# Kernel optimization log

Hardware: AMD Instinct MI355X
Metric: run time of the kernel (lower is better)

The kernel has to match this reference:

```python
import jax, jax.numpy as jnp
import numpy as np

B, CIN, COUT, H, W = 8, 256, 256, 64, 64
K, STRIDE, PAD = 3, 1, 1


def setup_inputs() -> dict:
    key = jax.random.key(0)
    k1, k2, k3 = jax.random.split(key, 3)
    x = jax.random.normal(k1, (B, CIN, H, W), dtype=jnp.float32)
    offset = jax.random.normal(k2, (B, 2 * K * K, H, W), dtype=jnp.float32)
    weight = jax.random.normal(k3, (COUT, CIN, K, K), dtype=jnp.float32) * 0.05
    return {"x": x, "offset": offset, "weight": weight}


def _deform_conv2d(x, offset, weight):
    # x: [B, C, H, W]; offset: [B, 2*K*K, Ho, Wo] (y,x interleaved per tap, mmcv layout)
    Bn, C, Hh, Ww = x.shape
    Ho, Wo = Hh, Ww  # stride=1, pad=1, k=3
    K2 = K * K
    ki, kj = jnp.meshgrid(jnp.arange(K), jnp.arange(K), indexing="ij")
    ki = ki.reshape(-1).astype(jnp.float32)  # [K2] row offset of tap
    kj = kj.reshape(-1).astype(jnp.float32)
    hh = jnp.arange(Ho, dtype=jnp.float32)
    ww = jnp.arange(Wo, dtype=jnp.float32)
    # base sampling grid per tap: [K2, Ho, Wo]
    base_y = ki[:, None, None] + hh[None, :, None] * STRIDE - PAD
    base_x = kj[:, None, None] + ww[None, None, :] * STRIDE - PAD
    off = offset.reshape(Bn, K2, 2, Ho, Wo)
    py = base_y[None] + off[:, :, 0]  # [B, K2, Ho, Wo]
    px = base_x[None] + off[:, :, 1]

    y0 = jnp.floor(py)
    x0 = jnp.floor(px)

    def gather(im, yy, xx):
        # im: [C, H, W]; yy, xx: [K2, Ho, Wo] -> [C, K2, Ho, Wo]
        return im[:, yy, xx]

    vgather = jax.vmap(gather)  # over batch

    val = jnp.zeros((Bn, C, K2, Ho, Wo), dtype=x.dtype)
    for dy in (0.0, 1.0):
        for dx in (0.0, 1.0):
            yi = y0 + dy
            xi = x0 + dx
            wgt = (1.0 - jnp.abs(py - yi)) * (1.0 - jnp.abs(px - xi))
            valid = (yi >= 0) & (yi < Hh) & (xi >= 0) & (xi < Ww)
            yc = jnp.clip(yi, 0, Hh - 1).astype(jnp.int32)
            xc = jnp.clip(xi, 0, Ww - 1).astype(jnp.int32)
            v = vgather(x, yc, xc)  # [B, C, K2, Ho, Wo]
            val = val + v * (wgt * valid)[:, None]

    w2 = weight.reshape(weight.shape[0], C, K2)
    return jnp.einsum("bckhw,ock->bohw", val, w2)


def reference(x, offset, weight):
    return jax.nn.relu(_deform_conv2d(x, offset, weight))
```

## Files before the change

### kernel.cpp

```cpp
#include <hip/hip_runtime.h>


#define B_   8
#define C_   256
#define H_   64
#define W_   64
#define K2_  9
#define HW_  4096
#define NC4  64

typedef __fp16 f16x2 __attribute__((ext_vector_type(2)));
typedef __fp16 f16x8 __attribute__((ext_vector_type(8)));
typedef float  f32x4 __attribute__((ext_vector_type(4)));

static __device__ __forceinline__ f16x2 u2h(unsigned u) {
    union { unsigned u; f16x2 h; } v; v.u = u; return v.h;
}
static __device__ __forceinline__ unsigned h2u(f16x2 h) {
    union { unsigned u; f16x2 h; } v; v.h = h; return v.u;
}

__global__ __launch_bounds__(256) void pack_kernel(
    const float* __restrict__ x, const float* __restrict__ w,
    uint4* __restrict__ xpt, unsigned short* __restrict__ wA)
{
    const int tid = threadIdx.x;
    if (blockIdx.x >= 512) {
        const int t = (blockIdx.x - 512) * 256 + tid;
        if (t < C_ * C_ * K2_) {
            const int k = t % 9;
            const int c = (t / 9) & 255;
            const int o = t / (9 * 256);
            const int cc = c >> 5, lg = (c >> 3) & 3, e = c & 7;
            const int t16 = o >> 4, lr = o & 15;
            const int dst = e + 8 * (lr + 16 * (lg + 4 * (t16 + 16 * (cc + 8 * k))));
            const __fp16 h = (__fp16)w[t];
            unsigned short us;
            __builtin_memcpy(&us, &h, 2);
            wA[dst] = us;
        }
        return;
    }
    const int bid = blockIdx.x;
    const int b = bid >> 6, y = bid & 63;
    __shared__ unsigned pr[64][256];
    const float* xb = x + ((size_t)(b * C_ + tid) * H_ + y) * W_;
#pragma unroll
    for (int i = 0; i < 16; ++i) {
        const int c0 = i * 4;
        const float4 v = *(const float4*)(xb + c0);
        const float nxt = xb[(c0 == 60) ? 63 : c0 + 4];
        pr[c0 + 0][tid] = h2u(__builtin_amdgcn_cvt_pkrtz(v.x, v.y));
        pr[c0 + 1][tid] = h2u(__builtin_amdgcn_cvt_pkrtz(v.y, v.z));
        pr[c0 + 2][tid] = h2u(__builtin_amdgcn_cvt_pkrtz(v.z, v.w));
        pr[c0 + 3][tid] = h2u(__builtin_amdgcn_cvt_pkrtz(v.w, nxt));
    }
    __syncthreads();
    const int lane = tid & 63, wv = tid >> 6;
    uint4* dst = xpt + ((size_t)b * HW_ + (size_t)y * 64) * NC4;
#pragma unroll
    for (int i = 0; i < 16; ++i) {
        const int col = wv * 16 + i;
        dst[(size_t)col * NC4 + lane] = *(const uint4*)&pr[col][lane * 4];
    }
}

template<int MODE>
__global__ __launch_bounds__(512, 2) void deform_main(
    const float* __restrict__ x, const uint4* __restrict__ xpt,
    const float* __restrict__ offset, const unsigned short* __restrict__ wA,
    float* __restrict__ out)
{
    extern __shared__ char smem[];
    unsigned short (*btile)[128][256] =
        (unsigned short (*)[128][256])smem;
    uint2*          gw2   = (uint2*)(smem + 131072);
    unsigned short* gaddr = (unsigned short*)(smem + 140288);

    const int bid = blockIdx.x;
    const int b = bid & 7, ho2 = bid >> 3;
    const int tid = threadIdx.x;
    const int lane = tid & 63;
    const int wv   = tid >> 6;
    const int lr = lane & 15, lg = (lane >> 4) & 3;

    for (int e = tid; e < K2_ * 128; e += 512) {
        const int k = e >> 7, p = e & 127;
        const int row = p >> 6, wo = p & 63;
        const int ho = ho2 * 2 + row;
        const float offy = offset[((b * 18 + 2 * k    ) * H_ + ho) * W_ + wo];
        const float offx = offset[((b * 18 + 2 * k + 1) * H_ + ho) * W_ + wo];
        const float py = (float)(k / 3 + ho - 1) + offy;
        const float px = (float)(k % 3 + wo - 1) + offx;
        const float y0f = floorf(py), x0f = floorf(px);
        const int   y0 = (int)y0f,   x0 = (int)x0f;
        const float fy = py - y0f,   fx = px - x0f;
        const float wy0 = (y0 >= 0  && y0 < H_)     ? 1.f - fy : 0.f;
        const float wy1 = (y0 >= -1 && y0 < H_ - 1) ? fy       : 0.f;
        const float wx0 = (x0 >= 0  && x0 < W_)     ? 1.f - fx : 0.f;
        const float wx1 = (x0 >= -1 && x0 < W_ - 1) ? fx       : 0.f;
        const int ys = min(max(y0, 0), H_ - 2);
        const int xs = min(max(x0, 0), W_ - 2);
        const float qy0 = (ys == y0 ? wy0 : 0.f) + (ys == y0 + 1 ? wy1 : 0.f);
        const float qy1 = (ys + 1 == y0 ? wy0 : 0.f) + (ys + 1 == y0 + 1 ? wy1 : 0.f);
        const float qx0 = (xs == x0 ? wx0 : 0.f) + (xs == x0 + 1 ? wx1 : 0.f);
        const float qx1 = (xs + 1 == x0 ? wx0 : 0.f) + (xs + 1 == x0 + 1 ? wx1 : 0.f);
        gaddr[k * 128 + p] = (unsigned short)(ys * W_ + xs);
        gw2[k * 128 + p] = make_uint2(
            h2u(__builtin_amdgcn_cvt_pkrtz(qy0 * qx0, qy0 * qx1)),
            h2u(__builtin_amdgcn_cvt_pkrtz(qy1 * qx0, qy1 * qx1)));
    }
    __syncthreads();

    f32x4 acc[2][8];
#pragma unroll
    for (int m = 0; m < 2; ++m)
#pragma unroll
        for (int n = 0; n < 8; ++n) acc[m][n] = (f32x4)0.f;

    const __fp16* wAh = (const __fp16*)wA;
    const uint4* xptb = xpt + (size_t)b * HW_ * NC4;

#define A_LOAD(k_, cc_, AS, AT) {                                              \
    const __fp16* ap_ = wAh +                                                  \
        (((size_t)((k_) * 8 + (cc_)) * 16 + wv * 2) * 64 + lane) * 8;          \
    AS = *(const f16x8*)ap_;                                                   \
    AT = *(const f16x8*)(ap_ + 512); }

#define G_ISSUE(t_, j_, QT, QB) {                                              \
    const int qp_ = gaddr[(t_) * 128 + wv * 16 + (j_)];                        \
    QT = xptb[(size_t)qp_ * NC4 + lane];                                       \
    QB = xptb[(size_t)(qp_ + 64) * NC4 + lane]; }

#define G_CONSUME(t_, j_, QT, QB, SB) {                                        \
    const int p_ = wv * 16 + (j_);                                             \
    const uint2 wp_ = gw2[(t_) * 128 + p_];                                    \
    const f16x2 wt_ = u2h(wp_.x), wb_ = u2h(wp_.y);                            \
    const float v0_ = __builtin_amdgcn_fdot2(u2h(QT.x), wt_,                   \
        __builtin_amdgcn_fdot2(u2h(QB.x), wb_, 0.f, false), false);            \
    const float v1_ = __builtin_amdgcn_fdot2(u2h(QT.y), wt_,                   \
        __builtin_amdgcn_fdot2(u2h(QB.y), wb_, 0.f, false), false);            \
    const float v2_ = __builtin_amdgcn_fdot2(u2h(QT.z), wt_,                   \
        __builtin_amdgcn_fdot2(u2h(QB.z), wb_, 0.f, false), false);            \
    const float v3_ = __builtin_amdgcn_fdot2(u2h(QT.w), wt_,                   \
        __builtin_amdgcn_fdot2(u2h(QB.w), wb_, 0.f, false), false);            \
    const unsigned pk0_ = h2u(__builtin_amdgcn_cvt_pkrtz(v0_, v1_));           \
    const unsigned pk1_ = h2u(__builtin_amdgcn_cvt_pkrtz(v2_, v3_));           \
    const int phys_ = (lane >> 1) ^ (p_ & 7);                                  \
    *(uint2*)((char*)&btile[SB][p_][0] + phys_ * 16 + (lane & 1) * 8) =        \
        make_uint2(pk0_, pk1_); }

#define MFMA_CC(cc_, MB, AS, AT) {                                             \
    _Pragma("unroll")                                                          \
    for (int nt = 0; nt < 8; ++nt) {                                           \
        const int pix_ = nt * 16 + lr;                                         \
        const int phys_ = ((cc_) * 4 + lg) ^ (pix_ & 7);                       \
        const f16x8 bv_ = *(const f16x8*)                                      \
            ((const char*)&btile[MB][pix_][0] + phys_ * 16);                   \
        acc[0][nt] = __builtin_amdgcn_mfma_f32_16x16x32_f16(                   \
            AS, bv_, acc[0][nt], 0, 0, 0);                                     \
        acc[1][nt] = __builtin_amdgcn_mfma_f32_16x16x32_f16(                   \
            AT, bv_, acc[1][nt], 0, 0, 0);                                     \
    } }

#define G_ISSUE_8(t_)                                                          \
    G_ISSUE(t_, 0, qT0, qB0) G_ISSUE(t_, 1, qT1, qB1)                          \
    G_ISSUE(t_, 2, qT2, qB2) G_ISSUE(t_, 3, qT3, qB3)                          \
    G_ISSUE(t_, 4, qT4, qB4) G_ISSUE(t_, 5, qT5, qB5)                          \
    G_ISSUE(t_, 6, qT6, qB6) G_ISSUE(t_, 7, qT7, qB7)

    if constexpr (MODE == 0) {
        uint4 qT0, qB0, qT1, qB1, qT2, qB2, qT3, qB3;
        uint4 qT4, qB4, qT5, qB5, qT6, qB6, qT7, qB7;
        f16x8 aS0, aT0, aS1, aT1, aS2, aT2, aS3, aT3;

        A_LOAD(0, 0, aS0, aT0)
        A_LOAD(0, 1, aS1, aT1)
        G_ISSUE_8(0)
        G_CONSUME(0, 0, qT0, qB0, 0)  G_ISSUE(0, 8, qT0, qB0)
        G_CONSUME(0, 1, qT1, qB1, 0)  G_ISSUE(0, 9, qT1, qB1)
        G_CONSUME(0, 2, qT2, qB2, 0)  G_ISSUE(0, 10, qT2, qB2)
        G_CONSUME(0, 3, qT3, qB3, 0)  G_ISSUE(0, 11, qT3, qB3)
        G_CONSUME(0, 4, qT4, qB4, 0)  G_ISSUE(0, 12, qT4, qB4)
        G_CONSUME(0, 5, qT5, qB5, 0)  G_ISSUE(0, 13, qT5, qB5)
        G_CONSUME(0, 6, qT6, qB6, 0)  G_ISSUE(0, 14, qT6, qB6)
        G_CONSUME(0, 7, qT7, qB7, 0)  G_ISSUE(0, 15, qT7, qB7)
        G_CONSUME(0, 8, qT0, qB0, 0)  G_CONSUME(0, 9, qT1, qB1, 0)
        G_CONSUME(0, 10, qT2, qB2, 0) G_CONSUME(0, 11, qT3, qB3, 0)
        G_CONSUME(0, 12, qT4, qB4, 0) G_CONSUME(0, 13, qT5, qB5, 0)
        G_CONSUME(0, 14, qT6, qB6, 0) G_CONSUME(0, 15, qT7, qB7, 0)
        G_ISSUE_8(1)
        asm volatile("s_waitcnt lgkmcnt(0)" ::: "memory");
        __builtin_amdgcn_s_barrier();

        for (int k = 0; k < K2_; ++k) {
            const int mb = k & 1, sb = mb ^ 1;
            const int st = (k < K2_ - 1);
            const int kn = st ? (k + 1) : k;

            A_LOAD(k, 2, aS2, aT2)
            if (st) { G_CONSUME(kn, 0, qT0, qB0, sb) G_ISSUE(kn, 8, qT0, qB0) }
            MFMA_CC(0, mb, aS0, aT0)
            A_LOAD(k, 3, aS3, aT3)
            if (st) { G_CONSUME(kn, 1, qT1, qB1, sb) G_ISSUE(kn, 9, qT1, qB1) }
            MFMA_CC(1, mb, aS1, aT1)
            A_LOAD(k, 4, aS0, aT0)
            if (st) { G_CONSUME(kn, 2, qT2, qB2, sb) G_ISSUE(kn, 10, qT2, qB2) }
            MFMA_CC(2, mb, aS2, aT2)
            A_LOAD(k, 5, aS1, aT1)
            if (st) { G_CONSUME(kn, 3, qT3, qB3, sb) G_ISSUE(kn, 11, qT3, qB3) }
            MFMA_CC(3, mb, aS3, aT3)
            A_LOAD(k, 6, aS2, aT2)
            if (st) { G_CONSUME(kn, 4, qT4, qB4, sb) G_ISSUE(kn, 12, qT4, qB4) }
            MFMA_CC(4, mb, aS0, aT0)
            A_LOAD(k, 7, aS3, aT3)
            if (st) { G_CONSUME(kn, 5, qT5, qB5, sb) G_ISSUE(kn, 13, qT5, qB5) }
            MFMA_CC(5, mb, aS1, aT1)
            if (st) {
                A_LOAD(kn, 0, aS0, aT0)
                A_LOAD(kn, 1, aS1, aT1)
                G_CONSUME(kn, 6, qT6, qB6, sb) G_ISSUE(kn, 14, qT6, qB6)
            }
            MFMA_CC(6, mb, aS2, aT2)
            if (st) { G_CONSUME(kn, 7, qT7, qB7, sb) G_ISSUE(kn, 15, qT7, qB7) }
            MFMA_CC(7, mb, aS3, aT3)
            if (st) {
                G_CONSUME(kn, 8, qT0, qB0, sb)  G_CONSUME(kn, 9, qT1, qB1, sb)
                G_CONSUME(kn, 10, qT2, qB2, sb) G_CONSUME(kn, 11, qT3, qB3, sb)
                G_CONSUME(kn, 12, qT4, qB4, sb) G_CONSUME(kn, 13, qT5, qB5, sb)
                G_CONSUME(kn, 14, qT6, qB6, sb) G_CONSUME(kn, 15, qT7, qB7, sb)
                if (k < K2_ - 2) { G_ISSUE_8(k + 2) }
            }
            asm volatile("s_waitcnt lgkmcnt(0)" ::: "memory");
            __builtin_amdgcn_s_barrier();
        }
    } else {
        for (int k = 0; k < K2_; ++k) {
#pragma unroll
            for (int j = 0; j < 16; ++j) {
                const int p_ = wv * 16 + j;
                const int qp = gaddr[k * 128 + p_];
                const uint2 wp_ = gw2[k * 128 + p_];
                const f16x2 wt_ = u2h(wp_.x), wb_ = u2h(wp_.y);
                const float w00 = (float)wt_.x, w01 = (float)wt_.y;
                const float w10 = (float)wb_.x, w11 = (float)wb_.y;
                float vv[4];
#pragma unroll
                for (int e2 = 0; e2 < 4; ++e2) {
                    const float* pl = x + ((size_t)(b * C_ + lane * 4 + e2)) * HW_;
                    vv[e2] = w00 * pl[qp] + w01 * pl[qp + 1]
                           + w10 * pl[qp + 64] + w11 * pl[qp + 65];
                }
                const unsigned pk0 = h2u(__builtin_amdgcn_cvt_pkrtz(vv[0], vv[1]));
                const unsigned pk1 = h2u(__builtin_amdgcn_cvt_pkrtz(vv[2], vv[3]));
                const int phys_ = (lane >> 1) ^ (p_ & 7);
                *(uint2*)((char*)&btile[0][p_][0] + phys_ * 16 + (lane & 1) * 8) =
                    make_uint2(pk0, pk1);
            }
            __syncthreads();
#pragma unroll
            for (int cc = 0; cc < 8; ++cc) {
                f16x8 a0, a1;
                A_LOAD(k, cc, a0, a1)
                MFMA_CC(cc, 0, a0, a1)
            }
            __syncthreads();
        }
    }

    const size_t ob = (size_t)b * C_ * HW_;
    const int hbase = ho2 * 2;
#pragma unroll
    for (int mt = 0; mt < 2; ++mt) {
        const int o0 = wv * 32 + mt * 16 + lg * 4;
#pragma unroll
        for (int nt = 0; nt < 8; ++nt) {
            const int pix = nt * 16 + lr;
            const int row = pix >> 6, wo = pix & 63;
#pragma unroll
            for (int r = 0; r < 4; ++r)
                out[ob + (size_t)(o0 + r) * HW_ + (size_t)(hbase + row) * W_ + wo] =
                    fmaxf(acc[mt][nt][r], 0.f);
        }
    }
#undef A_LOAD
#undef G_ISSUE
#undef G_CONSUME
#undef MFMA_CC
#undef G_ISSUE_8
}

extern "C" void kernel_launch(void* const* d_in, const int* in_sizes, int n_in,
                              void* d_out, int out_size, void* d_ws, size_t ws_size,
                              hipStream_t stream) {
    const float* x      = (const float*)d_in[0];
    const float* offset = (const float*)d_in[1];
    const float* weight = (const float*)d_in[2];
    float* out          = (float*)d_out;

    const size_t wA_bytes = (size_t)K2_ * C_ * C_ * 2;
    const size_t xp_off   = wA_bytes;
    const size_t xp_bytes = (size_t)B_ * HW_ * NC4 * 16;
    const size_t need     = xp_off + xp_bytes;

    unsigned short* wAp = (unsigned short*)d_ws;
    uint4*          xpp = (uint4*)((char*)d_ws + xp_off);

    pack_kernel<<<512 + 2304, 256, 0, stream>>>(x, weight, xpp, wAp);

    const size_t lds = 131072 + 9216 + 2304;
    if (ws_size >= need) {
        deform_main<0><<<256, 512, lds, stream>>>(x, xpp, offset, wAp, out);
    } else {
        deform_main<1><<<256, 512, lds, stream>>>(x, xpp, offset, wAp, out);
    }
}
```

Baseline: 72.35 us.

## Retile MFMA warp layout to 4x4 output-channel by pixel blocks

Changes each wave's MFMA tile from 32 output channels by 128 pixels to 64 output channels by 64 pixels, so waves form a 4x2 grid over channels and pixel rows. This halves the B-tile LDS reads per wave while doubling the weight (A) fragment loads from global memory. The A-load prefetch schedule is reworked into double-buffered groups of four fragments, and the epilogue store indexing is updated to match. Register pressure stays about the same.

Result: slower. 78.11 us (+8.0%).

```diff
diff --git a/kernel.cpp b/kernel.cpp
--- a/kernel.cpp
+++ b/kernel.cpp
@@ -83,6 +83,8 @@
     const int lane = tid & 63;
     const int wv   = tid >> 6;
     const int lr = lane & 15, lg = (lane >> 4) & 3;
+    const int mrow  = wv & 3;
+    const int npart = wv >> 2;
 
     for (int e = tid; e < K2_ * 128; e += 512) {
         const int k = e >> 7, p = e & 127;
@@ -112,20 +114,22 @@
     }
     __syncthreads();
 
-    f32x4 acc[2][8];
-#pragma unroll
-    for (int m = 0; m < 2; ++m)
-#pragma unroll
-        for (int n = 0; n < 8; ++n) acc[m][n] = (f32x4)0.f;
+    f32x4 acc[4][4];
+#pragma unroll
+    for (int m = 0; m < 4; ++m)
+#pragma unroll
+        for (int n = 0; n < 4; ++n) acc[m][n] = (f32x4)0.f;
 
     const __fp16* wAh = (const __fp16*)wA;
     const uint4* xptb = xpt + (size_t)b * HW_ * NC4;
 
-#define A_LOAD(k_, cc_, AS, AT) {                                              \
+#define A_LOAD4(k_, cc_, A0, A1, A2, A3) {                                     \
     const __fp16* ap_ = wAh +                                                  \
-        (((size_t)((k_) * 8 + (cc_)) * 16 + wv * 2) * 64 + lane) * 8;          \
-    AS = *(const f16x8*)ap_;                                                   \
-    AT = *(const f16x8*)(ap_ + 512); }
+        (((size_t)((k_) * 8 + (cc_)) * 16 + mrow * 4) * 64 + lane) * 8;        \
+    A0 = *(const f16x8*)ap_;                                                   \
+    A1 = *(const f16x8*)(ap_ + 512);                                           \
+    A2 = *(const f16x8*)(ap_ + 1024);                                          \
+    A3 = *(const f16x8*)(ap_ + 1536); }
 
 #define G_ISSUE(t_, j_, QT, QB) {                                              \
     const int qp_ = gaddr[(t_) * 128 + wv * 16 + (j_)];                        \
@@ -150,17 +154,21 @@
     *(uint2*)((char*)&btile[SB][p_][0] + phys_ * 16 + (lane & 1) * 8) =        \
         make_uint2(pk0_, pk1_); }
 
-#define MFMA_CC(cc_, MB, AS, AT) {                                             \
+#define MFMA_CC(cc_, MB, A0, A1, A2, A3) {                                     \
     _Pragma("unroll")                                                          \
-    for (int nt = 0; nt < 8; ++nt) {                                           \
-        const int pix_ = nt * 16 + lr;                                         \
+    for (int nt = 0; nt < 4; ++nt) {                                           \
+        const int pix_ = npart * 64 + nt * 16 + lr;                            \
         const int phys_ = ((cc_) * 4 + lg) ^ (pix_ & 7);                       \
         const f16x8 bv_ = *(const f16x8*)                                      \
             ((const char*)&btile[MB][pix_][0] + phys_ * 16);                   \
         acc[0][nt] = __builtin_amdgcn_mfma_f32_16x16x32_f16(                   \
-            AS, bv_, acc[0][nt], 0, 0, 0);                                     \
+            A0, bv_, acc[0][nt], 0, 0, 0);                                     \
         acc[1][nt] = __builtin_amdgcn_mfma_f32_16x16x32_f16(                   \
-            AT, bv_, acc[1][nt], 0, 0, 0);                                     \
+            A1, bv_, acc[1][nt], 0, 0, 0);                                     \
+        acc[2][nt] = __builtin_amdgcn_mfma_f32_16x16x32_f16(                   \
+            A2, bv_, acc[2][nt], 0, 0, 0);                                     \
+        acc[3][nt] = __builtin_amdgcn_mfma_f32_16x16x32_f16(                   \
+            A3, bv_, acc[3][nt], 0, 0, 0);                                     \
     } }
 
 #define G_ISSUE_8(t_)                                                          \
@@ -172,10 +180,10 @@
     if constexpr (MODE == 0) {
         uint4 qT0, qB0, qT1, qB1, qT2, qB2, qT3, qB3;
         uint4 qT4, qB4, qT5, qB5, qT6, qB6, qT7, qB7;
-        f16x8 aS0, aT0, aS1, aT1, aS2, aT2, aS3, aT3;
-
-        A_LOAD(0, 0, aS0, aT0)
-        A_LOAD(0, 1, aS1, aT1)
+        f16x8 aA0, aA1, aA2, aA3;
+        f16x8 aB0, aB1, aB2, aB3;
+
+        A_LOAD4(0, 0, aA0, aA1, aA2, aA3)
         G_ISSUE_8(0)
         G_CONSUME(0, 0, qT0, qB0, 0)  G_ISSUE(0, 8, qT0, qB0)
         G_CONSUME(0, 1, qT1, qB1, 0)  G_ISSUE(0, 9, qT1, qB1)
@@ -198,32 +206,32 @@
             const int st = (k < K2_ - 1);
             const int kn = st ? (k + 1) : k;
 
-            A_LOAD(k, 2, aS2, aT2)
+            A_LOAD4(k, 1, aB0, aB1, aB2, aB3)
             if (st) { G_CONSUME(kn, 0, qT0, qB0, sb) G_ISSUE(kn, 8, qT0, qB0) }
-            MFMA_CC(0, mb, aS0, aT0)
-            A_LOAD(k, 3, aS3, aT3)
+            MFMA_CC(0, mb, aA0, aA1, aA2, aA3)
+            A_LOAD4(k, 2, aA0, aA1, aA2, aA3)
             if (st) { G_CONSUME(kn, 1, qT1, qB1, sb) G_ISSUE(kn, 9, qT1, qB1) }
-            MFMA_CC(1, mb, aS1, aT1)
-            A_LOAD(k, 4, aS0, aT0)
+            MFMA_CC(1, mb, aB0, aB1, aB2, aB3)
+            A_LOAD4(k, 3, aB0, aB1, aB2, aB3)
             if (st) { G_CONSUME(kn, 2, qT2, qB2, sb) G_ISSUE(kn, 10, qT2, qB2) }
-            MFMA_CC(2, mb, aS2, aT2)
-            A_LOAD(k, 5, aS1, aT1)
+            MFMA_CC(2, mb, aA0, aA1, aA2, aA3)
+            A_LOAD4(k, 4, aA0, aA1, aA2, aA3)
             if (st) { G_CONSUME(kn, 3, qT3, qB3, sb) G_ISSUE(kn, 11, qT3, qB3) }
-            MFMA_CC(3, mb, aS3, aT3)
-            A_LOAD(k, 6, aS2, aT2)
+            MFMA_CC(3, mb, aB0, aB1, aB2, aB3)
+            A_LOAD4(k, 5, aB0, aB1, aB2, aB3)
             if (st) { G_CONSUME(kn, 4, qT4, qB4, sb) G_ISSUE(kn, 12, qT4, qB4) }
-            MFMA_CC(4, mb, aS0, aT0)
-            A_LOAD(k, 7, aS3, aT3)
+            MFMA_CC(4, mb, aA0, aA1, aA2, aA3)
+            A_LOAD4(k, 6, aA0, aA1, aA2, aA3)
             if (st) { G_CONSUME(kn, 5, qT5, qB5, sb) G_ISSUE(kn, 13, qT5, qB5) }
-            MFMA_CC(5, mb, aS1, aT1)
+            MFMA_CC(5, mb, aB0, aB1, aB2, aB3)
+            A_LOAD4(k, 7, aB0, aB1, aB2, aB3)
+            if (st) { G_CONSUME(kn, 6, qT6, qB6, sb) G_ISSUE(kn, 14, qT6, qB6) }
+            MFMA_CC(6, mb, aA0, aA1, aA2, aA3)
             if (st) {
-                A_LOAD(kn, 0, aS0, aT0)
-                A_LOAD(kn, 1, aS1, aT1)
-                G_CONSUME(kn, 6, qT6, qB6, sb) G_ISSUE(kn, 14, qT6, qB6)
+                A_LOAD4(kn, 0, aA0, aA1, aA2, aA3)
+                G_CONSUME(kn, 7, qT7, qB7, sb) G_ISSUE(kn, 15, qT7, qB7)
             }
-            MFMA_CC(6, mb, aS2, aT2)
-            if (st) { G_CONSUME(kn, 7, qT7, qB7, sb) G_ISSUE(kn, 15, qT7, qB7) }
-            MFMA_CC(7, mb, aS3, aT3)
+            MFMA_CC(7, mb, aB0, aB1, aB2, aB3)
             if (st) {
                 G_CONSUME(kn, 8, qT0, qB0, sb)  G_CONSUME(kn, 9, qT1, qB1, sb)
                 G_CONSUME(kn, 10, qT2, qB2, sb) G_CONSUME(kn, 11, qT3, qB3, sb)
@@ -260,9 +268,9 @@
             __syncthreads();
 #pragma unroll
             for (int cc = 0; cc < 8; ++cc) {
-                f16x8 a0, a1;
-                A_LOAD(k, cc, a0, a1)
-                MFMA_CC(cc, 0, a0, a1)
+                f16x8 a0, a1, a2, a3;
+                A_LOAD4(k, cc, a0, a1, a2, a3)
+                MFMA_CC(cc, 0, a0, a1, a2, a3)
             }
             __syncthreads();
         }
@@ -271,19 +279,19 @@
     const size_t ob = (size_t)b * C_ * HW_;
     const int hbase = ho2 * 2;
 #pragma unroll
-    for (int mt = 0; mt < 2; ++mt) {
-        const int o0 = wv * 32 + mt * 16 + lg * 4;
-#pragma unroll
-        for (int nt = 0; nt < 8; ++nt) {
-            const int pix = nt * 16 + lr;
-            const int row = pix >> 6, wo = pix & 63;
+    for (int mt = 0; mt < 4; ++mt) {
+        const int o0 = mrow * 64 + mt * 16 + lg * 4;
+#pragma unroll
+        for (int nt = 0; nt < 4; ++nt) {
+            const int wo = nt * 16 + lr;
 #pragma unroll
             for (int r = 0; r < 4; ++r)
-                out[ob + (size_t)(o0 + r) * HW_ + (size_t)(hbase + row) * W_ + wo] =
+                out[ob + (size_t)(o0 + r) * HW_
+                    + (size_t)(hbase + npart) * W_ + wo] =
                     fmaxf(acc[mt][nt][r], 0.f);
         }
     }
-#undef A_LOAD
+#undef A_LOAD4
 #undef G_ISSUE
 #undef G_CONSUME
 #undef MFMA_CC
```

## Split waves into MFMA-first and gather-first groups to stagger pipeline phases

Applied to the files above, without the earlier changes.

Each k-step used to interleave gather consume/issue with MFMA work inside every wave. Now half the waves (wv&4) run all their MFMAs first and then the next stage's gather, while the other half gather first and then run MFMAs. The goal is for the two groups to keep the matrix units and the memory/VALU path busy at the same time within a CU. The trade-off is that each wave loses its own fine-grained overlap, and the wave-divergent branch may increase code size or register pressure.

Result: slower. 76.73 us (+6.1%).

```diff
diff --git a/kernel.cpp b/kernel.cpp
--- a/kernel.cpp
+++ b/kernel.cpp
@@ -169,6 +169,22 @@
     G_ISSUE(t_, 4, qT4, qB4) G_ISSUE(t_, 5, qT5, qB5)                          \
     G_ISSUE(t_, 6, qT6, qB6) G_ISSUE(t_, 7, qT7, qB7)
 
+#define STAGE_HEAD(kn_, sb_)                                                   \
+    G_CONSUME(kn_, 0, qT0, qB0, sb_) G_ISSUE(kn_, 8, qT0, qB0)                 \
+    G_CONSUME(kn_, 1, qT1, qB1, sb_) G_ISSUE(kn_, 9, qT1, qB1)                 \
+    G_CONSUME(kn_, 2, qT2, qB2, sb_) G_ISSUE(kn_, 10, qT2, qB2)                \
+    G_CONSUME(kn_, 3, qT3, qB3, sb_) G_ISSUE(kn_, 11, qT3, qB3)                \
+    G_CONSUME(kn_, 4, qT4, qB4, sb_) G_ISSUE(kn_, 12, qT4, qB4)                \
+    G_CONSUME(kn_, 5, qT5, qB5, sb_) G_ISSUE(kn_, 13, qT5, qB5)                \
+    G_CONSUME(kn_, 6, qT6, qB6, sb_) G_ISSUE(kn_, 14, qT6, qB6)                \
+    G_CONSUME(kn_, 7, qT7, qB7, sb_) G_ISSUE(kn_, 15, qT7, qB7)
+
+#define STAGE_TAIL(kn_, sb_)                                                   \
+    G_CONSUME(kn_, 8, qT0, qB0, sb_)  G_CONSUME(kn_, 9, qT1, qB1, sb_)         \
+    G_CONSUME(kn_, 10, qT2, qB2, sb_) G_CONSUME(kn_, 11, qT3, qB3, sb_)        \
+    G_CONSUME(kn_, 12, qT4, qB4, sb_) G_CONSUME(kn_, 13, qT5, qB5, sb_)        \
+    G_CONSUME(kn_, 14, qT6, qB6, sb_) G_CONSUME(kn_, 15, qT7, qB7, sb_)
+
     if constexpr (MODE == 0) {
         uint4 qT0, qB0, qT1, qB1, qT2, qB2, qT3, qB3;
         uint4 qT4, qB4, qT5, qB5, qT6, qB6, qT7, qB7;
@@ -177,59 +193,53 @@
         A_LOAD(0, 0, aS0, aT0)
         A_LOAD(0, 1, aS1, aT1)
         G_ISSUE_8(0)
-        G_CONSUME(0, 0, qT0, qB0, 0)  G_ISSUE(0, 8, qT0, qB0)
-        G_CONSUME(0, 1, qT1, qB1, 0)  G_ISSUE(0, 9, qT1, qB1)
-        G_CONSUME(0, 2, qT2, qB2, 0)  G_ISSUE(0, 10, qT2, qB2)
-        G_CONSUME(0, 3, qT3, qB3, 0)  G_ISSUE(0, 11, qT3, qB3)
-        G_CONSUME(0, 4, qT4, qB4, 0)  G_ISSUE(0, 12, qT4, qB4)
-        G_CONSUME(0, 5, qT5, qB5, 0)  G_ISSUE(0, 13, qT5, qB5)
-        G_CONSUME(0, 6, qT6, qB6, 0)  G_ISSUE(0, 14, qT6, qB6)
-        G_CONSUME(0, 7, qT7, qB7, 0)  G_ISSUE(0, 15, qT7, qB7)
-        G_CONSUME(0, 8, qT0, qB0, 0)  G_CONSUME(0, 9, qT1, qB1, 0)
-        G_CONSUME(0, 10, qT2, qB2, 0) G_CONSUME(0, 11, qT3, qB3, 0)
-        G_CONSUME(0, 12, qT4, qB4, 0) G_CONSUME(0, 13, qT5, qB5, 0)
-        G_CONSUME(0, 14, qT6, qB6, 0) G_CONSUME(0, 15, qT7, qB7, 0)
+        STAGE_HEAD(0, 0)
+        STAGE_TAIL(0, 0)
         G_ISSUE_8(1)
         asm volatile("s_waitcnt lgkmcnt(0)" ::: "memory");
         __builtin_amdgcn_s_barrier();
+
+        const bool mfma_first = (wv & 4) != 0;
 
         for (int k = 0; k < K2_; ++k) {
             const int mb = k & 1, sb = mb ^ 1;
             const int st = (k < K2_ - 1);
             const int kn = st ? (k + 1) : k;
 
-            A_LOAD(k, 2, aS2, aT2)
-            if (st) { G_CONSUME(kn, 0, qT0, qB0, sb) G_ISSUE(kn, 8, qT0, qB0) }
-            MFMA_CC(0, mb, aS0, aT0)
-            A_LOAD(k, 3, aS3, aT3)
-            if (st) { G_CONSUME(kn, 1, qT1, qB1, sb) G_ISSUE(kn, 9, qT1, qB1) }
-            MFMA_CC(1, mb, aS1, aT1)
-            A_LOAD(k, 4, aS0, aT0)
-            if (st) { G_CONSUME(kn, 2, qT2, qB2, sb) G_ISSUE(kn, 10, qT2, qB2) }
-            MFMA_CC(2, mb, aS2, aT2)
-            A_LOAD(k, 5, aS1, aT1)
-            if (st) { G_CONSUME(kn, 3, qT3, qB3, sb) G_ISSUE(kn, 11, qT3, qB3) }
-            MFMA_CC(3, mb, aS3, aT3)
-            A_LOAD(k, 6, aS2, aT2)
-            if (st) { G_CONSUME(kn, 4, qT4, qB4, sb) G_ISSUE(kn, 12, qT4, qB4) }
-            MFMA_CC(4, mb, aS0, aT0)
-            A_LOAD(k, 7, aS3, aT3)
-            if (st) { G_CONSUME(kn, 5, qT5, qB5, sb) G_ISSUE(kn, 13, qT5, qB5) }
-            MFMA_CC(5, mb, aS1, aT1)
-            if (st) {
-                A_LOAD(kn, 0, aS0, aT0)
-                A_LOAD(kn, 1, aS1, aT1)
-                G_CONSUME(kn, 6, qT6, qB6, sb) G_ISSUE(kn, 14, qT6, qB6)
-            }
-            MFMA_CC(6, mb, aS2, aT2)
-            if (st) { G_CONSUME(kn, 7, qT7, qB7, sb) G_ISSUE(kn, 15, qT7, qB7) }
-            MFMA_CC(7, mb, aS3, aT3)
-            if (st) {
-                G_CONSUME(kn, 8, qT0, qB0, sb)  G_CONSUME(kn, 9, qT1, qB1, sb)
-                G_CONSUME(kn, 10, qT2, qB2, sb) G_CONSUME(kn, 11, qT3, qB3, sb)
-                G_CONSUME(kn, 12, qT4, qB4, sb) G_CONSUME(kn, 13, qT5, qB5, sb)
-                G_CONSUME(kn, 14, qT6, qB6, sb) G_CONSUME(kn, 15, qT7, qB7, sb)
-                if (k < K2_ - 2) { G_ISSUE_8(k + 2) }
+            if (mfma_first) {
+                A_LOAD(k, 2, aS2, aT2) MFMA_CC(0, mb, aS0, aT0)
+                A_LOAD(k, 3, aS3, aT3) MFMA_CC(1, mb, aS1, aT1)
+                A_LOAD(k, 4, aS0, aT0) MFMA_CC(2, mb, aS2, aT2)
+                A_LOAD(k, 5, aS1, aT1) MFMA_CC(3, mb, aS3, aT3)
+                A_LOAD(k, 6, aS2, aT2) MFMA_CC(4, mb, aS0, aT0)
+                A_LOAD(k, 7, aS3, aT3) MFMA_CC(5, mb, aS1, aT1)
+                MFMA_CC(6, mb, aS2, aT2)
+                MFMA_CC(7, mb, aS3, aT3)
+                if (st) {
+                    STAGE_HEAD(kn, sb)
+                    A_LOAD(kn, 0, aS0, aT0)
+                    A_LOAD(kn, 1, aS1, aT1)
+                    STAGE_TAIL(kn, sb)
+                    if (k < K2_ - 2) { G_ISSUE_8(k + 2) }
+                }
+            } else {
+                if (st) {
+                    STAGE_HEAD(kn, sb)
+                    STAGE_TAIL(kn, sb)
+                    if (k < K2_ - 2) { G_ISSUE_8(k + 2) }
+                }
+                A_LOAD(k, 2, aS2, aT2) MFMA_CC(0, mb, aS0, aT0)
+                A_LOAD(k, 3, aS3, aT3) MFMA_CC(1, mb, aS1, aT1)
+                A_LOAD(k, 4, aS0, aT0) MFMA_CC(2, mb, aS2, aT2)
+                A_LOAD(k, 5, aS1, aT1) MFMA_CC(3, mb, aS3, aT3)
+                A_LOAD(k, 6, aS2, aT2) MFMA_CC(4, mb, aS0, aT0)
+                A_LOAD(k, 7, aS3, aT3) MFMA_CC(5, mb, aS1, aT1)
+                if (st) {
+                    A_LOAD(kn, 0, aS0, aT0)
+                    A_LOAD(kn, 1, aS1, aT1)
+                }
+                MFMA_CC(6, mb, aS2, aT2)
+                MFMA_CC(7, mb, aS3, aT3)
             }
             asm volatile("s_waitcnt lgkmcnt(0)" ::: "memory");
             __builtin_amdgcn_s_barrier();
@@ -288,6 +298,8 @@
 #undef G_CONSUME
 #undef MFMA_CC
 #undef G_ISSUE_8
+#undef STAGE_HEAD
+#undef STAGE_TAIL
 }
 
 extern "C" void kernel_launch(void* const* d_in, const int* in_sizes, int n_in,
```

## Single-buffer the B tile in LDS and raise launch bounds to four blocks

Applied to the files above, without the earlier changes.

Shrinks the LDS B tile from a double buffer to a single buffer, roughly halving shared memory per block, and raises the launch-bounds occupancy hint from 2 to 4 blocks. The main loop changes from overlapping the gather and interpolate stage for tap k+1 with the MFMAs of tap k to a sequential schedule. Global gathers for the next tap are issued during the MFMAs, then the tile is built after a barrier. With only 256 blocks launched, higher occupancy may not help, and the tighter register budget plus the lost overlap and extra barrier per tap could hurt.

After: 278.8 us. +285.4%, slower.

```diff
diff --git a/kernel.cpp b/kernel.cpp
--- a/kernel.cpp
+++ b/kernel.cpp
@@ -66,16 +66,16 @@
 }
 
 template<int MODE>
-__global__ __launch_bounds__(512, 2) void deform_main(
+__global__ __launch_bounds__(512, 4) void deform_main(
     const float* __restrict__ x, const uint4* __restrict__ xpt,
     const float* __restrict__ offset, const unsigned short* __restrict__ wA,
     float* __restrict__ out)
 {
     extern __shared__ char smem[];
-    unsigned short (*btile)[128][256] =
-        (unsigned short (*)[128][256])smem;
-    uint2*          gw2   = (uint2*)(smem + 131072);
-    unsigned short* gaddr = (unsigned short*)(smem + 140288);
+    unsigned short (*btile)[256] =
+        (unsigned short (*)[256])smem;
+    uint2*          gw2   = (uint2*)(smem + 65536);
+    unsigned short* gaddr = (unsigned short*)(smem + 74752);
 
     const int bid = blockIdx.x;
     const int b = bid & 7, ho2 = bid >> 3;
@@ -132,7 +132,7 @@
     QT = xptb[(size_t)qp_ * NC4 + lane];                                       \
     QB = xptb[(size_t)(qp_ + 64) * NC4 + lane]; }
 
-#define G_CONSUME(t_, j_, QT, QB, SB) {                                        \
+#define G_CONSUME(t_, j_, QT, QB) {                                            \
     const int p_ = wv * 16 + (j_);                                             \
     const uint2 wp_ = gw2[(t_) * 128 + p_];                                    \
     const f16x2 wt_ = u2h(wp_.x), wb_ = u2h(wp_.y);                            \
@@ -147,16 +147,16 @@
     const unsigned pk0_ = h2u(__builtin_amdgcn_cvt_pkrtz(v0_, v1_));           \
     const unsigned pk1_ = h2u(__builtin_amdgcn_cvt_pkrtz(v2_, v3_));           \
     const int phys_ = (lane >> 1) ^ (p_ & 7);                                  \
-    *(uint2*)((char*)&btile[SB][p_][0] + phys_ * 16 + (lane & 1) * 8) =        \
+    *(uint2*)((char*)&btile[p_][0] + phys_ * 16 + (lane & 1) * 8) =            \
         make_uint2(pk0_, pk1_); }
 
-#define MFMA_CC(cc_, MB, AS, AT) {                                             \
+#define MFMA_CC(cc_, AS, AT) {                                                 \
     _Pragma("unroll")                                                          \
     for (int nt = 0; nt < 8; ++nt) {                                           \
         const int pix_ = nt * 16 + lr;                                         \
         const int phys_ = ((cc_) * 4 + lg) ^ (pix_ & 7);                       \
         const f16x8 bv_ = *(const f16x8*)                                      \
-            ((const char*)&btile[MB][pix_][0] + phys_ * 16);                   \
+            ((const char*)&btile[pix_][0] + phys_ * 16);                       \
         acc[0][nt] = __builtin_amdgcn_mfma_f32_16x16x32_f16(                   \
             AS, bv_, acc[0][nt], 0, 0, 0);                                     \
         acc[1][nt] = __builtin_amdgcn_mfma_f32_16x16x32_f16(                   \
@@ -169,6 +169,20 @@
     G_ISSUE(t_, 4, qT4, qB4) G_ISSUE(t_, 5, qT5, qB5)                          \
     G_ISSUE(t_, 6, qT6, qB6) G_ISSUE(t_, 7, qT7, qB7)
 
+#define STAGE_FULL(t_)                                                         \
+    G_CONSUME(t_, 0, qT0, qB0)  G_ISSUE(t_, 8, qT0, qB0)                       \
+    G_CONSUME(t_, 1, qT1, qB1)  G_ISSUE(t_, 9, qT1, qB1)                       \
+    G_CONSUME(t_, 2, qT2, qB2)  G_ISSUE(t_, 10, qT2, qB2)                      \
+    G_CONSUME(t_, 3, qT3, qB3)  G_ISSUE(t_, 11, qT3, qB3)                      \
+    G_CONSUME(t_, 4, qT4, qB4)  G_ISSUE(t_, 12, qT4, qB4)                      \
+    G_CONSUME(t_, 5, qT5, qB5)  G_ISSUE(t_, 13, qT5, qB5)                      \
+    G_CONSUME(t_, 6, qT6, qB6)  G_ISSUE(t_, 14, qT6, qB6)                      \
+    G_CONSUME(t_, 7, qT7, qB7)  G_ISSUE(t_, 15, qT7, qB7)                      \
+    G_CONSUME(t_, 8, qT0, qB0)  G_CONSUME(t_, 9, qT1, qB1)                     \
+    G_CONSUME(t_, 10, qT2, qB2) G_CONSUME(t_, 11, qT3, qB3)                    \
+    G_CONSUME(t_, 12, qT4, qB4) G_CONSUME(t_, 13, qT5, qB5)                    \
+    G_CONSUME(t_, 14, qT6, qB6) G_CONSUME(t_, 15, qT7, qB7)
+
     if constexpr (MODE == 0) {
         uint4 qT0, qB0, qT1, qB1, qT2, qB2, qT3, qB3;
         uint4 qT4, qB4, qT5, qB5, qT6, qB6, qT7, qB7;
@@ -177,62 +191,35 @@
         A_LOAD(0, 0, aS0, aT0)
         A_LOAD(0, 1, aS1, aT1)
         G_ISSUE_8(0)
-        G_CONSUME(0, 0, qT0, qB0, 0)  G_ISSUE(0, 8, qT0, qB0)
-        G_CONSUME(0, 1, qT1, qB1, 0)  G_ISSUE(0, 9, qT1, qB1)
-        G_CONSUME(0, 2, qT2, qB2, 0)  G_ISSUE(0, 10, qT2, qB2)
-        G_CONSUME(0, 3, qT3, qB3, 0)  G_ISSUE(0, 11, qT3, qB3)
-        G_CONSUME(0, 4, qT4, qB4, 0)  G_ISSUE(0, 12, qT4, qB4)
-        G_CONSUME(0, 5, qT5, qB5, 0)  G_ISSUE(0, 13, qT5, qB5)
-        G_CONSUME(0, 6, qT6, qB6, 0)  G_ISSUE(0, 14, qT6, qB6)
-        G_CONSUME(0, 7, qT7, qB7, 0)  G_ISSUE(0, 15, qT7, qB7)
-        G_CONSUME(0, 8, qT0, qB0, 0)  G_CONSUME(0, 9, qT1, qB1, 0)
-        G_CONSUME(0, 10, qT2, qB2, 0) G_CONSUME(0, 11, qT3, qB3, 0)
-        G_CONSUME(0, 12, qT4, qB4, 0) G_CONSUME(0, 13, qT5, qB5, 0)
-        G_CONSUME(0, 14, qT6, qB6, 0) G_CONSUME(0, 15, qT7, qB7, 0)
-        G_ISSUE_8(1)
+        STAGE_FULL(0)
         asm volatile("s_waitcnt lgkmcnt(0)" ::: "memory");
         __builtin_amdgcn_s_barrier();
 
         for (int k = 0; k < K2_; ++k) {
-            const int mb = k & 1, sb = mb ^ 1;
             const int st = (k < K2_ - 1);
             const int kn = st ? (k + 1) : k;
 
-            A_LOAD(k, 2, aS2, aT2)
-            if (st) { G_CONSUME(kn, 0, qT0, qB0, sb) G_ISSUE(kn, 8, qT0, qB0) }
-            MFMA_CC(0, mb, aS0, aT0)
-            A_LOAD(k, 3, aS3, aT3)
-            if (st) { G_CONSUME(kn, 1, qT1, qB1, sb) G_ISSUE(kn, 9, qT1, qB1) }
-            MFMA_CC(1, mb, aS1, aT1)
-            A_LOAD(k, 4, aS0, aT0)
-            if (st) { G_CONSUME(kn, 2, qT2, qB2, sb) G_ISSUE(kn, 10, qT2, qB2) }
-            MFMA_CC(2, mb, aS2, aT2)
-            A_LOAD(k, 5, aS1, aT1)
-            if (st) { G_CONSUME(kn, 3, qT3, qB3, sb) G_ISSUE(kn, 11, qT3, qB3) }
-            MFMA_CC(3, mb, aS3, aT3)
-            A_LOAD(k, 6, aS2, aT2)
-            if (st) { G_CONSUME(kn, 4, qT4, qB4, sb) G_ISSUE(kn, 12, qT4, qB4) }
-            MFMA_CC(4, mb, aS0, aT0)
-            A_LOAD(k, 7, aS3, aT3)
-            if (st) { G_CONSUME(kn, 5, qT5, qB5, sb) G_ISSUE(kn, 13, qT5, qB5) }
-            MFMA_CC(5, mb, aS1, aT1)
+            A_LOAD(k, 2, aS2, aT2) MFMA_CC(0, aS0, aT0)
+            A_LOAD(k, 3, aS3, aT3) MFMA_CC(1, aS1, aT1)
+            A_LOAD(k, 4, aS0, aT0) MFMA_CC(2, aS2, aT2)
+            A_LOAD(k, 5, aS1, aT1) MFMA_CC(3, aS3, aT3)
+            A_LOAD(k, 6, aS2, aT2) MFMA_CC(4, aS0, aT0)
+            A_LOAD(k, 7, aS3, aT3) MFMA_CC(5, aS1, aT1)
             if (st) {
                 A_LOAD(kn, 0, aS0, aT0)
                 A_LOAD(kn, 1, aS1, aT1)
-                G_CONSUME(kn, 6, qT6, qB6, sb) G_ISSUE(kn, 14, qT6, qB6)
+                G_ISSUE_8(kn)
             }
-            MFMA_CC(6, mb, aS2, aT2)
-            if (st) { G_CONSUME(kn, 7, qT7, qB7, sb) G_ISSUE(kn, 15, qT7, qB7) }
-            MFMA_CC(7, mb, aS3, aT3)
-            if (st) {
-                G_CONSUME(kn, 8, qT0, qB0, sb)  G_CONSUME(kn, 9, qT1, qB1, sb)
-                G_CONSUME(kn, 10, qT2, qB2, sb) G_CONSUME(kn, 11, qT3, qB3, sb)
-                G_CONSUME(kn, 12, qT4, qB4, sb) G_CONSUME(kn, 13, qT5, qB5, sb)
-                G_CONSUME(kn, 14, qT6, qB6, sb) G_CONSUME(kn, 15, qT7, qB7, sb)
-                if (k < K2_ - 2) { G_ISSUE_8(k + 2) }
-            }
+            MFMA_CC(6, aS2, aT2)
+            MFMA_CC(7, aS3, aT3)
             asm volatile("s_waitcnt lgkmcnt(0)" ::: "memory");
             __builtin_amdgcn_s_barrier();
+
+            if (st) {
+                STAGE_FULL(kn)
+                asm volatile("s_waitcnt lgkmcnt(0)" ::: "memory");
+                __builtin_amdgcn_s_barrier();
+            }
         }
     } else {
         for (int k = 0; k < K2_; ++k) {
@@ -254,7 +241,7 @@
                 const unsigned pk0 = h2u(__builtin_amdgcn_cvt_pkrtz(vv[0], vv[1]));
                 const unsigned pk1 = h2u(__builtin_amdgcn_cvt_pkrtz(vv[2], vv[3]));
                 const int phys_ = (lane >> 1) ^ (p_ & 7);
-                *(uint2*)((char*)&btile[0][p_][0] + phys_ * 16 + (lane & 1) * 8) =
+                *(uint2*)((char*)&btile[p_][0] + phys_ * 16 + (lane & 1) * 8) =
                     make_uint2(pk0, pk1);
             }
             __syncthreads();
@@ -262,7 +249,7 @@
             for (int cc = 0; cc < 8; ++cc) {
                 f16x8 a0, a1;
                 A_LOAD(k, cc, a0, a1)
-                MFMA_CC(cc, 0, a0, a1)
+                MFMA_CC(cc, a0, a1)
             }
             __syncthreads();
         }
@@ -288,6 +275,7 @@
 #undef G_CONSUME
 #undef MFMA_CC
 #undef G_ISSUE_8
+#undef STAGE_FULL
 }
 
 extern "C" void kernel_launch(void* const* d_in, const int* in_sizes, int n_in,
@@ -308,7 +296,7 @@
 
     pack_kernel<<<512 + 2304, 256, 0, stream>>>(x, weight, xpp, wAp);
 
-    const size_t lds = 131072 + 9216 + 2304;
+    const size_t lds = 65536 + 9216 + 2304;
     if (ws_size >= need) {
         deform_main<0><<<256, 512, lds, stream>>>(x, xpp, offset, wAp, out);
     } else {
```
